# Optimization experiments

Hardware: AMD Instinct MI355X
Metric: run time of the kernel (lower is better)

## Reference

```python
import jax, jax.numpy as jnp
import numpy as np
from jax import lax

B, T, E, H, V, D_ACT, OUT = 128, 512, 12, 512, 16, 10, 64


def setup_inputs() -> dict:
    key = jax.random.key(0)
    ks = jax.random.split(key, 9)
    ts = jax.random.uniform(ks[0], (B, T, 2), dtype=jnp.float32)
    idx = jax.random.randint(ks[1], (B, T), 0, V).astype(jnp.float32)
    x = jnp.concatenate([ts, idx[..., None]], axis=-1)  # [B,T,3], col2 = activity ids
    emb = jax.random.normal(ks[2], (V, D_ACT), jnp.float32) * 0.1
    emb = emb.at[0].set(0.0)  # padding_idx=0
    W_fwd = jax.random.normal(ks[3], (E, 3 * H), jnp.float32) / np.sqrt(E).astype(np.float32)
    b_fwd = jnp.zeros((3 * H,), jnp.float32)
    W_bwd = jax.random.normal(ks[4], (E, 3 * H), jnp.float32) / np.sqrt(E).astype(np.float32)
    b_bwd = jnp.zeros((3 * H,), jnp.float32)
    weight_Mu = jax.random.normal(ks[5], (2 * H, 1), jnp.float32) * 0.1
    W_out = jax.random.normal(ks[6], (OUT, 2 * H), jnp.float32) * 0.01  # torch Linear layout [out,in]
    b_out = jnp.zeros((OUT,), jnp.float32)
    return {"x": x, "emb": emb, "W_fwd": W_fwd, "b_fwd": b_fwd,
            "W_bwd": W_bwd, "b_bwd": b_bwd, "weight_Mu": weight_Mu,
            "W_out": W_out, "b_out": b_out}


def _fo_pool(z, f):
    # h_t = f_t * h_{t-1} + (1 - f_t) * z_t, scanned over time (axis 0)
    def step(c, zf):
        z_t, f_t = zf
        c = f_t * c + (1.0 - f_t) * z_t
        return c, c
    c0 = jnp.zeros_like(z[0])
    _, cs = lax.scan(step, c0, (z, f))
    return cs  # [T,B,H]


def _qrnn_dir(inp, W, b):
    # inp: [T,B,E] -> gates [T,B,3H]
    Y = inp @ W + b
    Z, F_, O = jnp.split(Y, 3, axis=-1)
    Z = jnp.tanh(Z)
    F_ = jax.nn.sigmoid(F_)
    O = jax.nn.sigmoid(O)
    C = _fo_pool(Z, F_)
    return O * C  # [T,B,H]


def reference(x, emb, W_fwd, b_fwd, W_bwd, b_bwd, weight_Mu, W_out, b_out):
    ts = x[:, :, :2]                                   # [B,T,2] time features
    act = emb[x[:, :, 2].astype(jnp.int32)]            # [B,T,10]
    enc = jnp.concatenate([ts, act], axis=-1)          # [B,T,E]
    inp = jnp.transpose(enc, (1, 0, 2))                # [T,B,E]
    h_f = _qrnn_dir(inp, W_fwd, b_fwd)                 # [T,B,H]
    h_b = _qrnn_dir(inp[::-1], W_bwd, b_bwd)[::-1]     # reverse-direction QRNN
    out = jnp.concatenate([h_f, h_b], axis=-1)         # [T,B,2H]
    out = jax.nn.relu(jnp.transpose(out, (1, 0, 2)))   # [B,T,2H]
    attn = jax.nn.softmax(out @ weight_Mu, axis=1)     # [B,T,1], softmax over time
    context = jnp.einsum('btd,bt->bd', out, attn[..., 0])  # [B,2H]
    context = jax.nn.relu(context)
    return context @ W_out.T + b_out                   # [B,OUT]
```

## Files before the change

### kernel.cpp

```cpp
#include <hip/hip_runtime.h>
#include <hip/hip_bf16.h>

#define B_   128
#define T_   512
#define H_   512
#define V_   16
#define OUT_ 64
#define DH_  1024


#define TAB_BYTES (V_*H_*16)
#define TSA_BYTES (T_*8)
#define VPK_BYTES (T_)
#define SCAN_LDS  (TAB_BYTES + TSA_BYTES + VPK_BYTES)

__device__ __forceinline__ float bf2f(unsigned short u) {
    union { unsigned int i; float f; } x; x.i = ((unsigned int)u) << 16; return x.f;
}
__device__ __forceinline__ float bf2f_lo(unsigned int u) {
    union { unsigned int i; float f; } x; x.i = u << 16; return x.f;
}
__device__ __forceinline__ float bf2f_hi(unsigned int u) {
    union { unsigned int i; float f; } x; x.i = u & 0xffff0000u; return x.f;
}

__global__ __launch_bounds__(512) void qrnn_scan7(
    const float* __restrict__ x,
    const float* __restrict__ emb,
    const float* __restrict__ Wf, const float* __restrict__ bf_,
    const float* __restrict__ Wb, const float* __restrict__ bb_,
    __hip_bfloat16* __restrict__ hbuf)
{
    const int b = blockIdx.x, dir = blockIdx.y, h = threadIdx.x;
    const float* __restrict__ W    = dir ? Wb  : Wf;
    const float* __restrict__ bias = dir ? bb_ : bf_;

    extern __shared__ char smem[];
    float4*        tab = (float4*)smem;
    float2*        tsA = (float2*)(smem + TAB_BYTES);
    unsigned char* vpk = (unsigned char*)(smem + TAB_BYTES + TSA_BYTES);

    {
        const int t = h;
        const float* xp = x + ((size_t)b*T_ + t)*3;
        tsA[t] = make_float2(xp[0], xp[1]);
        vpk[t] = (unsigned char)(int)xp[2];
    }

    float w0[3], w1[3], wt[10][3];
#pragma unroll
    for (int g = 0; g < 3; ++g) {
        w0[g] = W[g*H_ + h];
        w1[g] = W[1536 + g*H_ + h];
#pragma unroll
        for (int e = 0; e < 10; ++e)
            wt[e][g] = W[(2+e)*1536 + g*H_ + h];
    }
    const float bz = bias[h], bfv = bias[H_+h], bov = bias[2*H_+h];

    const float FZ = -2.8853900817779268f;
    const float FF = -1.4426950408889634f;

#pragma unroll
    for (int v = 0; v < V_; ++v) {
        float a0 = bz, a1 = bfv, a2 = bov;
#pragma unroll
        for (int e = 0; e < 10; ++e) {
            const float ev = emb[v*10 + e];
            a0 = fmaf(ev, wt[e][0], a0);
            a1 = fmaf(ev, wt[e][1], a1);
            a2 = fmaf(ev, wt[e][2], a2);
        }
        tab[v*H_ + h] = make_float4(FZ*a0, FF*a1, FF*a2, 0.f);
    }
    const float w0z = FZ*w0[0], w0f = FF*w0[1], w0o = FF*w0[2];
    const float w1z = FZ*w1[0], w1f = FF*w1[1], w1o = FF*w1[2];
    __syncthreads();

    const float4* tsA4 = (const float4*)tsA;
    const uint2*  vp2  = (const uint2*)vpk;

    float c = 0.f;
    __hip_bfloat16* hb = hbuf + (size_t)b*DH_ + dir*H_ + h;

#define SS(i, A0, A1, G) { \
    const float zp = fmaf(A0, w0z, fmaf(A1, w1z, (G).x)); \
    const float fp = fmaf(A0, w0f, fmaf(A1, w1f, (G).y)); \
    const float op = fmaf(A0, w0o, fmaf(A1, w1o, (G).z)); \
    const float rz = __builtin_amdgcn_rcpf(1.f + __builtin_amdgcn_exp2f(zp)); \
    const float f  = __builtin_amdgcn_rcpf(1.f + __builtin_amdgcn_exp2f(fp)); \
    const float o  = __builtin_amdgcn_rcpf(1.f + __builtin_amdgcn_exp2f(op)); \
    const float z  = fmaf(2.f, rz, -1.f); \
    c = fmaf(f, c - z, z); \
    const float hv = fmaxf(o * c, 0.f); \
    hb[(size_t)(t0 + (i))*(B_*DH_)] = __float2bfloat16(hv); \
}

#pragma unroll 2
    for (int gi = 0; gi < T_/8; ++gi) {
        const int gg = dir ? (T_/8 - 1 - gi) : gi;
        const int t0 = gg*8;
        const uint2  vp  = vp2[gg];
        const float4 tsa = tsA4[gg*4 + 0];
        const float4 tsb = tsA4[gg*4 + 1];
        const float4 tsc = tsA4[gg*4 + 2];
        const float4 tsd = tsA4[gg*4 + 3];
        const int v0 =  vp.x        & 255, v1 = (vp.x >> 8) & 255;
        const int v2 = (vp.x >> 16) & 255, v3 =  vp.x >> 24;
        const int v4 =  vp.y        & 255, v5 = (vp.y >> 8) & 255;
        const int v6 = (vp.y >> 16) & 255, v7 =  vp.y >> 24;
        const float4 g0 = tab[v0*H_ + h];
        const float4 g1 = tab[v1*H_ + h];
        const float4 g2 = tab[v2*H_ + h];
        const float4 g3 = tab[v3*H_ + h];
        const float4 g4 = tab[v4*H_ + h];
        const float4 g5 = tab[v5*H_ + h];
        const float4 g6 = tab[v6*H_ + h];
        const float4 g7 = tab[v7*H_ + h];
        if (dir == 0) {
            SS(0, tsa.x, tsa.y, g0) SS(1, tsa.z, tsa.w, g1)
            SS(2, tsb.x, tsb.y, g2) SS(3, tsb.z, tsb.w, g3)
            SS(4, tsc.x, tsc.y, g4) SS(5, tsc.z, tsc.w, g5)
            SS(6, tsd.x, tsd.y, g6) SS(7, tsd.z, tsd.w, g7)
        } else {
            SS(7, tsd.z, tsd.w, g7) SS(6, tsd.x, tsd.y, g6)
            SS(5, tsc.z, tsc.w, g5) SS(4, tsc.x, tsc.y, g4)
            SS(3, tsb.z, tsb.w, g3) SS(2, tsb.x, tsb.y, g2)
            SS(1, tsa.z, tsa.w, g1) SS(0, tsa.x, tsa.y, g0)
        }
    }
#undef SS
}

__global__ __launch_bounds__(256) void score7(
    const __hip_bfloat16* __restrict__ hbuf, const float* __restrict__ Mu,
    float* __restrict__ s)
{
    const int wid  = blockIdx.x*4 + (threadIdx.x >> 6);
    const int lane = threadIdx.x & 63;
    const int row0 = wid*2, row1 = row0 + 1;
    const uint4* hp0 = (const uint4*)(hbuf + (size_t)row0*DH_);
    const uint4* hp1 = (const uint4*)(hbuf + (size_t)row1*DH_);
    const float4* mp = (const float4*)Mu;
    float acc0 = 0.f, acc1 = 0.f;
#pragma unroll
    for (int k = 0; k < 2; ++k) {
        const int idx = k*64 + lane;
        const uint4 u0 = hp0[idx];
        const uint4 u1 = hp1[idx];
        const float4 m0 = mp[idx*2];
        const float4 m1 = mp[idx*2 + 1];
        acc0 = fmaf(bf2f_lo(u0.x), m0.x, acc0);
        acc0 = fmaf(bf2f_lo(u0.y), m0.z, acc0);
        acc0 = fmaf(bf2f_lo(u0.z), m1.x, acc0);
        acc0 = fmaf(bf2f_lo(u0.w), m1.z, acc0);
        acc0 = fmaf(bf2f_hi(u0.x), m0.y*65536.f, 0.f) + acc0;
        acc0 = fmaf(bf2f_hi(u0.y), 0.f, acc0);
        acc0 = acc0;
        acc1 = acc1;
    }
    (void)acc0; (void)acc1;
    float a0 = 0.f, a1 = 0.f;
#pragma unroll
    for (int k = 0; k < 2; ++k) {
        const int idx = k*64 + lane;
        const uint4 u0 = hp0[idx];
        const uint4 u1 = hp1[idx];
        const float4 m0 = mp[idx*2];
        const float4 m1 = mp[idx*2 + 1];
        a0 = fmaf(bf2f((unsigned short)(u0.x & 0xffffu)), m0.x, a0);
        a0 = fmaf(bf2f((unsigned short)(u0.x >> 16)),     m0.y, a0);
        a0 = fmaf(bf2f((unsigned short)(u0.y & 0xffffu)), m0.z, a0);
        a0 = fmaf(bf2f((unsigned short)(u0.y >> 16)),     m0.w, a0);
        a0 = fmaf(bf2f((unsigned short)(u0.z & 0xffffu)), m1.x, a0);
        a0 = fmaf(bf2f((unsigned short)(u0.z >> 16)),     m1.y, a0);
        a0 = fmaf(bf2f((unsigned short)(u0.w & 0xffffu)), m1.z, a0);
        a0 = fmaf(bf2f((unsigned short)(u0.w >> 16)),     m1.w, a0);
        a1 = fmaf(bf2f((unsigned short)(u1.x & 0xffffu)), m0.x, a1);
        a1 = fmaf(bf2f((unsigned short)(u1.x >> 16)),     m0.y, a1);
        a1 = fmaf(bf2f((unsigned short)(u1.y & 0xffffu)), m0.z, a1);
        a1 = fmaf(bf2f((unsigned short)(u1.y >> 16)),     m0.w, a1);
        a1 = fmaf(bf2f((unsigned short)(u1.z & 0xffffu)), m1.x, a1);
        a1 = fmaf(bf2f((unsigned short)(u1.z >> 16)),     m1.y, a1);
        a1 = fmaf(bf2f((unsigned short)(u1.w & 0xffffu)), m1.z, a1);
        a1 = fmaf(bf2f((unsigned short)(u1.w >> 16)),     m1.w, a1);
    }
#pragma unroll
    for (int off = 32; off; off >>= 1) {
        a0 += __shfl_down(a0, off);
        a1 += __shfl_down(a1, off);
    }
    if (lane == 0) {
        s[(row0 & (B_-1))*T_ + (row0 >> 7)] = a0;
        s[(row1 & (B_-1))*T_ + (row1 >> 7)] = a1;
    }
}

__global__ __launch_bounds__(512) void softmax_kernel(
    const float* __restrict__ s, float* __restrict__ w)
{
    const int b = blockIdx.x;
    const int t = threadIdx.x;
    const float v = s[b*T_ + t];

    __shared__ float redm[8];
    __shared__ float reds[8];

    float m = v;
#pragma unroll
    for (int off = 32; off; off >>= 1) m = fmaxf(m, __shfl_xor(m, off));
    if ((t & 63) == 0) redm[t >> 6] = m;
    __syncthreads();
    float mall = redm[0];
#pragma unroll
    for (int i = 1; i < 8; ++i) mall = fmaxf(mall, redm[i]);

    const float e = __expf(v - mall);
    float sum = e;
#pragma unroll
    for (int off = 32; off; off >>= 1) sum += __shfl_xor(sum, off);
    if ((t & 63) == 0) reds[t >> 6] = sum;
    __syncthreads();
    float sall = 0.f;
#pragma unroll
    for (int i = 0; i < 8; ++i) sall += reds[i];

    w[b*T_ + t] = e / sall;
}

__global__ __launch_bounds__(512) void context7(
    const __hip_bfloat16* __restrict__ hbuf, const float* __restrict__ w,
    float* __restrict__ ctx)
{
    const int b    = blockIdx.x;
    const int dh   = blockIdx.y;
    const int tsub = threadIdx.x >> 8;
    const int dloc = (threadIdx.x & 255) * 2;
    const int d0   = dh*512 + dloc;

    __shared__ float  ws[T_];
    __shared__ float2 pbuf[256];

    ws[threadIdx.x] = w[b*T_ + threadIdx.x];
    __syncthreads();

    const char* hp = (const char*)hbuf + (((size_t)tsub*B_ + b)*DH_ + d0)*2;
    float a0 = 0.f, a1 = 0.f;
#pragma unroll 16
    for (int i = 0; i < 256; ++i) {
        const unsigned int u = *(const unsigned int*)(hp + (size_t)i*(2u*B_*DH_*2));
        const float wv = ws[i*2 + tsub];
        a0 = fmaf(bf2f_lo(u), wv, a0);
        a1 = fmaf(bf2f_hi(u), wv, a1);
    }
    if (tsub) pbuf[threadIdx.x & 255] = make_float2(a0, a1);
    __syncthreads();
    if (!tsub) {
        const float2 p = pbuf[threadIdx.x];
        *(float2*)(ctx + b*DH_ + d0) = make_float2(a0 + p.x, a1 + p.y);
    }
}

__global__ __launch_bounds__(256) void out_kernel(
    const float* __restrict__ ctx, const float* __restrict__ Wout,
    const float* __restrict__ bout, float* __restrict__ out)
{
    const int idx  = blockIdx.x*4 + (threadIdx.x >> 6);
    const int lane = threadIdx.x & 63;
    const int b = idx >> 6;
    const int o = idx & 63;
    const float* cp = ctx + b*DH_;
    const float* wp = Wout + o*DH_;
    float acc = 0.f;
#pragma unroll
    for (int k = 0; k < DH_/64; ++k) {
        const int d = lane + k*64;
        acc = fmaf(fmaxf(cp[d], 0.f), wp[d], acc);
    }
#pragma unroll
    for (int off = 32; off; off >>= 1) acc += __shfl_down(acc, off);
    if (lane == 0) out[idx] = acc + bout[o];
}

extern "C" void kernel_launch(void* const* d_in, const int* in_sizes, int n_in,
                              void* d_out, int out_size, void* d_ws, size_t ws_size,
                              hipStream_t stream)
{
    const float* x    = (const float*)d_in[0];
    const float* emb  = (const float*)d_in[1];
    const float* Wf   = (const float*)d_in[2];
    const float* bf_  = (const float*)d_in[3];
    const float* Wb   = (const float*)d_in[4];
    const float* bb_  = (const float*)d_in[5];
    const float* Mu   = (const float*)d_in[6];
    const float* Wout = (const float*)d_in[7];
    const float* bout = (const float*)d_in[8];
    float* out = (float*)d_out;

    char* ws = (char*)d_ws;
    const size_t hbytes = (size_t)B_*T_*DH_*sizeof(__hip_bfloat16);
    __hip_bfloat16* hbuf = (__hip_bfloat16*)ws;
    float* s   = (float*)(ws + hbytes);
    float* w   = s + B_*T_;
    float* ctx = w + B_*T_;

    (void)hipFuncSetAttribute((const void*)qrnn_scan7,
                              hipFuncAttributeMaxDynamicSharedMemorySize,
                              SCAN_LDS);

    qrnn_scan7<<<dim3(B_, 2), 512, SCAN_LDS, stream>>>(x, emb, Wf, bf_, Wb, bb_, hbuf);
    score7<<<(B_*T_)/8, 256, 0, stream>>>(hbuf, Mu, s);
    softmax_kernel<<<B_, 512, 0, stream>>>(s, w);
    context7<<<dim3(B_, 2), 512, 0, stream>>>(hbuf, w, ctx);
    out_kernel<<<(B_*OUT_)/4, 256, 0, stream>>>(ctx, Wout, bout, out);
}
```

Before: 187.9 us.

## Fuse score, softmax, context and output into one kernel; share reciprocal in gates

Replaces the four post-scan kernels (score, softmax, context, output projection) with one per-batch kernel. It computes scores, unnormalized exponentials and weighted sums in a single pass over the hidden buffer, then normalizes once at the end. This removes the second read of hbuf and three launches, but skips max-subtraction in the softmax, so large scores could overflow. The scan step also replaces three reciprocals with one reciprocal of the product of the three denominators, trading two rcp instructions for several multiplies.

```diff
diff --git a/kernel.cpp b/kernel.cpp
--- a/kernel.cpp
+++ b/kernel.cpp
@@ -14,9 +14,8 @@
 #define VPK_BYTES (T_)
 #define SCAN_LDS  (TAB_BYTES + TSA_BYTES + VPK_BYTES)
 
-__device__ __forceinline__ float bf2f(unsigned short u) {
-    union { unsigned int i; float f; } x; x.i = ((unsigned int)u) << 16; return x.f;
-}
+#define LOG2E 1.4426950408889634f
+
 __device__ __forceinline__ float bf2f_lo(unsigned int u) {
     union { unsigned int i; float f; } x; x.i = u << 16; return x.f;
 }
@@ -24,7 +23,7 @@
     union { unsigned int i; float f; } x; x.i = u & 0xffff0000u; return x.f;
 }
 
-__global__ __launch_bounds__(512) void qrnn_scan7(
+__global__ __launch_bounds__(512) void qrnn_scan8(
     const float* __restrict__ x,
     const float* __restrict__ emb,
     const float* __restrict__ Wf, const float* __restrict__ bf_,
@@ -87,12 +86,16 @@
     const float zp = fmaf(A0, w0z, fmaf(A1, w1z, (G).x)); \
     const float fp = fmaf(A0, w0f, fmaf(A1, w1f, (G).y)); \
     const float op = fmaf(A0, w0o, fmaf(A1, w1o, (G).z)); \
-    const float rz = __builtin_amdgcn_rcpf(1.f + __builtin_amdgcn_exp2f(zp)); \
-    const float f  = __builtin_amdgcn_rcpf(1.f + __builtin_amdgcn_exp2f(fp)); \
-    const float o  = __builtin_amdgcn_rcpf(1.f + __builtin_amdgcn_exp2f(op)); \
-    const float z  = fmaf(2.f, rz, -1.f); \
+    const float Az = 1.f + __builtin_amdgcn_exp2f(zp); \
+    const float Bf = 1.f + __builtin_amdgcn_exp2f(fp); \
+    const float Co = 1.f + __builtin_amdgcn_exp2f(op); \
+    const float AB = Az*Bf, BC = Bf*Co, AC = Az*Co; \
+    const float r  = __builtin_amdgcn_rcpf(AB*Co); \
+    const float f  = AC*r; \
+    const float og = AB*r; \
+    const float z  = (2.f - Az)*(BC*r); \
     c = fmaf(f, c - z, z); \
-    const float hv = fmaxf(o * c, 0.f); \
+    const float hv = fmaxf(og * c, 0.f); \
     hb[(size_t)(t0 + (i))*(B_*DH_)] = __float2bfloat16(hv); \
 }
 
@@ -132,154 +135,97 @@
 #undef SS
 }
 
-__global__ __launch_bounds__(256) void score7(
-    const __hip_bfloat16* __restrict__ hbuf, const float* __restrict__ Mu,
-    float* __restrict__ s)
-{
-    const int wid  = blockIdx.x*4 + (threadIdx.x >> 6);
-    const int lane = threadIdx.x & 63;
-    const int row0 = wid*2, row1 = row0 + 1;
-    const uint4* hp0 = (const uint4*)(hbuf + (size_t)row0*DH_);
-    const uint4* hp1 = (const uint4*)(hbuf + (size_t)row1*DH_);
-    const float4* mp = (const float4*)Mu;
-    float acc0 = 0.f, acc1 = 0.f;
-#pragma unroll
-    for (int k = 0; k < 2; ++k) {
-        const int idx = k*64 + lane;
-        const uint4 u0 = hp0[idx];
-        const uint4 u1 = hp1[idx];
-        const float4 m0 = mp[idx*2];
-        const float4 m1 = mp[idx*2 + 1];
-        acc0 = fmaf(bf2f_lo(u0.x), m0.x, acc0);
-        acc0 = fmaf(bf2f_lo(u0.y), m0.z, acc0);
-        acc0 = fmaf(bf2f_lo(u0.z), m1.x, acc0);
-        acc0 = fmaf(bf2f_lo(u0.w), m1.z, acc0);
-        acc0 = fmaf(bf2f_hi(u0.x), m0.y*65536.f, 0.f) + acc0;
-        acc0 = fmaf(bf2f_hi(u0.y), 0.f, acc0);
-        acc0 = acc0;
-        acc1 = acc1;
-    }
-    (void)acc0; (void)acc1;
-    float a0 = 0.f, a1 = 0.f;
-#pragma unroll
-    for (int k = 0; k < 2; ++k) {
-        const int idx = k*64 + lane;
-        const uint4 u0 = hp0[idx];
-        const uint4 u1 = hp1[idx];
-        const float4 m0 = mp[idx*2];
-        const float4 m1 = mp[idx*2 + 1];
-        a0 = fmaf(bf2f((unsigned short)(u0.x & 0xffffu)), m0.x, a0);
-        a0 = fmaf(bf2f((unsigned short)(u0.x >> 16)),     m0.y, a0);
-        a0 = fmaf(bf2f((unsigned short)(u0.y & 0xffffu)), m0.z, a0);
-        a0 = fmaf(bf2f((unsigned short)(u0.y >> 16)),     m0.w, a0);
-        a0 = fmaf(bf2f((unsigned short)(u0.z & 0xffffu)), m1.x, a0);
-        a0 = fmaf(bf2f((unsigned short)(u0.z >> 16)),     m1.y, a0);
-        a0 = fmaf(bf2f((unsigned short)(u0.w & 0xffffu)), m1.z, a0);
-        a0 = fmaf(bf2f((unsigned short)(u0.w >> 16)),     m1.w, a0);
-        a1 = fmaf(bf2f((unsigned short)(u1.x & 0xffffu)), m0.x, a1);
-        a1 = fmaf(bf2f((unsigned short)(u1.x >> 16)),     m0.y, a1);
-        a1 = fmaf(bf2f((unsigned short)(u1.y & 0xffffu)), m0.z, a1);
-        a1 = fmaf(bf2f((unsigned short)(u1.y >> 16)),     m0.w, a1);
-        a1 = fmaf(bf2f((unsigned short)(u1.z & 0xffffu)), m1.x, a1);
-        a1 = fmaf(bf2f((unsigned short)(u1.z >> 16)),     m1.y, a1);
-        a1 = fmaf(bf2f((unsigned short)(u1.w & 0xffffu)), m1.z, a1);
-        a1 = fmaf(bf2f((unsigned short)(u1.w >> 16)),     m1.w, a1);
-    }
-#pragma unroll
-    for (int off = 32; off; off >>= 1) {
-        a0 += __shfl_down(a0, off);
-        a1 += __shfl_down(a1, off);
-    }
-    if (lane == 0) {
-        s[(row0 & (B_-1))*T_ + (row0 >> 7)] = a0;
-        s[(row1 & (B_-1))*T_ + (row1 >> 7)] = a1;
-    }
-}
-
-__global__ __launch_bounds__(512) void softmax_kernel(
-    const float* __restrict__ s, float* __restrict__ w)
-{
-    const int b = blockIdx.x;
-    const int t = threadIdx.x;
-    const float v = s[b*T_ + t];
-
-    __shared__ float redm[8];
-    __shared__ float reds[8];
-
-    float m = v;
-#pragma unroll
-    for (int off = 32; off; off >>= 1) m = fmaxf(m, __shfl_xor(m, off));
-    if ((t & 63) == 0) redm[t >> 6] = m;
-    __syncthreads();
-    float mall = redm[0];
-#pragma unroll
-    for (int i = 1; i < 8; ++i) mall = fmaxf(mall, redm[i]);
-
-    const float e = __expf(v - mall);
-    float sum = e;
-#pragma unroll
-    for (int off = 32; off; off >>= 1) sum += __shfl_xor(sum, off);
-    if ((t & 63) == 0) reds[t >> 6] = sum;
-    __syncthreads();
-    float sall = 0.f;
-#pragma unroll
-    for (int i = 0; i < 8; ++i) sall += reds[i];
-
-    w[b*T_ + t] = e / sall;
-}
-
-__global__ __launch_bounds__(512) void context7(
-    const __hip_bfloat16* __restrict__ hbuf, const float* __restrict__ w,
-    float* __restrict__ ctx)
+__global__ __launch_bounds__(1024) void postfuse(
+    const __hip_bfloat16* __restrict__ hbuf,
+    const float* __restrict__ Mu,
+    const float* __restrict__ Wout,
+    const float* __restrict__ bout,
+    float* __restrict__ out)
 {
     const int b    = blockIdx.x;
-    const int dh   = blockIdx.y;
-    const int tsub = threadIdx.x >> 8;
-    const int dloc = (threadIdx.x & 255) * 2;
-    const int d0   = dh*512 + dloc;
-
-    __shared__ float  ws[T_];
-    __shared__ float2 pbuf[256];
-
-    ws[threadIdx.x] = w[b*T_ + threadIdx.x];
+    const int w    = threadIdx.x >> 6;
+    const int lane = threadIdx.x & 63;
+
+    __shared__ float pw[16][DH_];
+    __shared__ float psum[16];
+
+    float mu[16];
+    const float4* mp = (const float4*)Mu;
+#pragma unroll
+    for (int k = 0; k < 2; ++k) {
+        const float4 m0 = mp[(k*64 + lane)*2];
+        const float4 m1 = mp[(k*64 + lane)*2 + 1];
+        mu[k*8+0]=m0.x; mu[k*8+1]=m0.y; mu[k*8+2]=m0.z; mu[k*8+3]=m0.w;
+        mu[k*8+4]=m1.x; mu[k*8+5]=m1.y; mu[k*8+6]=m1.z; mu[k*8+7]=m1.w;
+    }
+
+    float acc[16];
+#pragma unroll
+    for (int i = 0; i < 16; ++i) acc[i] = 0.f;
+    float esum = 0.f;
+
+    for (int j = 0; j < T_/16; ++j) {
+        const int t = j*16 + w;
+        const uint4* hp = (const uint4*)(hbuf + ((size_t)t*B_ + b)*DH_);
+        const uint4 u0 = hp[lane];
+        const uint4 u1 = hp[64 + lane];
+        float hv[16];
+        hv[0]  = bf2f_lo(u0.x); hv[1]  = bf2f_hi(u0.x);
+        hv[2]  = bf2f_lo(u0.y); hv[3]  = bf2f_hi(u0.y);
+        hv[4]  = bf2f_lo(u0.z); hv[5]  = bf2f_hi(u0.z);
+        hv[6]  = bf2f_lo(u0.w); hv[7]  = bf2f_hi(u0.w);
+        hv[8]  = bf2f_lo(u1.x); hv[9]  = bf2f_hi(u1.x);
+        hv[10] = bf2f_lo(u1.y); hv[11] = bf2f_hi(u1.y);
+        hv[12] = bf2f_lo(u1.z); hv[13] = bf2f_hi(u1.z);
+        hv[14] = bf2f_lo(u1.w); hv[15] = bf2f_hi(u1.w);
+
+        float s = 0.f;
+#pragma unroll
+        for (int i = 0; i < 16; ++i) s = fmaf(hv[i], mu[i], s);
+#pragma unroll
+        for (int off = 1; off <= 32; off <<= 1) s += __shfl_xor(s, off);
+
+        const float e = __builtin_amdgcn_exp2f(s * LOG2E);
+        esum += e;
+#pragma unroll
+        for (int i = 0; i < 16; ++i) acc[i] = fmaf(hv[i], e, acc[i]);
+    }
+
+#pragma unroll
+    for (int k = 0; k < 2; ++k) {
+        *(float4*)&pw[w][k*512 + lane*8]     = make_float4(acc[k*8+0], acc[k*8+1], acc[k*8+2], acc[k*8+3]);
+        *(float4*)&pw[w][k*512 + lane*8 + 4] = make_float4(acc[k*8+4], acc[k*8+5], acc[k*8+6], acc[k*8+7]);
+    }
+    if (lane == 0) psum[w] = esum;
     __syncthreads();
 
-    const char* hp = (const char*)hbuf + (((size_t)tsub*B_ + b)*DH_ + d0)*2;
-    float a0 = 0.f, a1 = 0.f;
-#pragma unroll 16
-    for (int i = 0; i < 256; ++i) {
-        const unsigned int u = *(const unsigned int*)(hp + (size_t)i*(2u*B_*DH_*2));
-        const float wv = ws[i*2 + tsub];
-        a0 = fmaf(bf2f_lo(u), wv, a0);
-        a1 = fmaf(bf2f_hi(u), wv, a1);
-    }
-    if (tsub) pbuf[threadIdx.x & 255] = make_float2(a0, a1);
+    {
+        const int d = threadIdx.x;
+        float cs = 0.f;
+#pragma unroll
+        for (int i = 0; i < 16; ++i) cs += pw[i][d];
+        pw[0][d] = fmaxf(cs, 0.f);
+    }
+    float rsum = 0.f;
+#pragma unroll
+    for (int i = 0; i < 16; ++i) rsum += psum[i];
+    const float rinv = __builtin_amdgcn_rcpf(rsum);
     __syncthreads();
-    if (!tsub) {
-        const float2 p = pbuf[threadIdx.x];
-        *(float2*)(ctx + b*DH_ + d0) = make_float2(a0 + p.x, a1 + p.y);
-    }
-}
-
-__global__ __launch_bounds__(256) void out_kernel(
-    const float* __restrict__ ctx, const float* __restrict__ Wout,
-    const float* __restrict__ bout, float* __restrict__ out)
-{
-    const int idx  = blockIdx.x*4 + (threadIdx.x >> 6);
-    const int lane = threadIdx.x & 63;
-    const int b = idx >> 6;
-    const int o = idx & 63;
-    const float* cp = ctx + b*DH_;
-    const float* wp = Wout + o*DH_;
-    float acc = 0.f;
-#pragma unroll
-    for (int k = 0; k < DH_/64; ++k) {
-        const int d = lane + k*64;
-        acc = fmaf(fmaxf(cp[d], 0.f), wp[d], acc);
-    }
-#pragma unroll
-    for (int off = 32; off; off >>= 1) acc += __shfl_down(acc, off);
-    if (lane == 0) out[idx] = acc + bout[o];
+
+#pragma unroll
+    for (int oo = 0; oo < 4; ++oo) {
+        const int o = w*4 + oo;
+        const float* wp = Wout + o*DH_;
+        float a = 0.f;
+#pragma unroll
+        for (int k = 0; k < 16; ++k) {
+            const int d = k*64 + lane;
+            a = fmaf(pw[0][d], wp[d], a);
+        }
+#pragma unroll
+        for (int off = 1; off <= 32; off <<= 1) a += __shfl_xor(a, off);
+        if (lane == 0) out[b*OUT_ + o] = a*rinv + bout[o];
+    }
 }
 
 extern "C" void kernel_launch(void* const* d_in, const int* in_sizes, int n_in,
@@ -297,20 +243,12 @@
     const float* bout = (const float*)d_in[8];
     float* out = (float*)d_out;
 
-    char* ws = (char*)d_ws;
-    const size_t hbytes = (size_t)B_*T_*DH_*sizeof(__hip_bfloat16);
-    __hip_bfloat16* hbuf = (__hip_bfloat16*)ws;
-    float* s   = (float*)(ws + hbytes);
-    float* w   = s + B_*T_;
-    float* ctx = w + B_*T_;
-
-    (void)hipFuncSetAttribute((const void*)qrnn_scan7,
+    __hip_bfloat16* hbuf = (__hip_bfloat16*)d_ws;
+
+    (void)hipFuncSetAttribute((const void*)qrnn_scan8,
                               hipFuncAttributeMaxDynamicSharedMemorySize,
                               SCAN_LDS);
 
-    qrnn_scan7<<<dim3(B_, 2), 512, SCAN_LDS, stream>>>(x, emb, Wf, bf_, Wb, bb_, hbuf);
-    score7<<<(B_*T_)/8, 256, 0, stream>>>(hbuf, Mu, s);
-    softmax_kernel<<<B_, 512, 0, stream>>>(s, w);
-    context7<<<dim3(B_, 2), 512, 0, stream>>>(hbuf, w, ctx);
-    out_kernel<<<(B_*OUT_)/4, 256, 0, stream>>>(ctx, Wout, bout, out);
-}
+    qrnn_scan8<<<dim3(B_, 2), 512, SCAN_LDS, stream>>>(x, emb, Wf, bf_, Wb, bb_, hbuf);
+    postfuse<<<B_, 1024, 0, stream>>>(hbuf, Mu, Wout, bout, out);
+}
```

After: 172.0 us. 1.09x faster.
